# Performance work log

Hardware: AMD Instinct MI355X
Metric: run time of the kernel (lower is better)

The kernel has to match this reference:

```python
import jax, jax.numpy as jnp
import numpy as np

N_NODES = 10000
IN_FEAT = 16
HID = 64
TCH = 32
B, W, E = 4, 12, 320000


def setup_inputs() -> dict:
    key = jax.random.key(0)
    ks = jax.random.split(key, 12)
    x = jax.random.normal(ks[0], (B, W, N_NODES, IN_FEAT), dtype=jnp.float32)
    edge_index = jax.random.randint(ks[1], (2, E), 0, N_NODES, dtype=jnp.int32)
    s = lambda fan: 1.0 / np.sqrt(fan)
    W1 = jax.random.uniform(ks[2], (IN_FEAT, HID), jnp.float32, -s(IN_FEAT), s(IN_FEAT))
    b1 = jnp.zeros((HID,), jnp.float32)
    W2 = jax.random.uniform(ks[3], (HID, HID), jnp.float32, -s(HID), s(HID))
    b2 = jnp.zeros((HID,), jnp.float32)
    conv1_w = jax.random.uniform(ks[4], (TCH, HID, 3), jnp.float32, -s(HID * 3), s(HID * 3))
    conv1_b = jax.random.uniform(ks[5], (TCH,), jnp.float32, -s(HID * 3), s(HID * 3))
    conv2_w = jax.random.uniform(ks[6], (TCH, TCH, 3), jnp.float32, -s(TCH * 3), s(TCH * 3))
    conv2_b = jax.random.uniform(ks[7], (TCH,), jnp.float32, -s(TCH * 3), s(TCH * 3))
    fc_w = jax.random.uniform(ks[8], (1, TCH), jnp.float32, -s(TCH), s(TCH))
    fc_b = jax.random.uniform(ks[9], (1,), jnp.float32, -s(TCH), s(TCH))
    return {"x": x, "edge_index": edge_index, "W1": W1, "b1": b1, "W2": W2,
            "b2": b2, "conv1_w": conv1_w, "conv1_b": conv1_b,
            "conv2_w": conv2_w, "conv2_b": conv2_b, "fc_w": fc_w, "fc_b": fc_b}


def _conv1d(h, w, b):
    # h: (BN, C_in, W), w: (C_out, C_in, K)
    out = jax.lax.conv_general_dilated(h, w, window_strides=(1,), padding=[(1, 1)],
                                       dimension_numbers=("NCH", "OIH", "NCH"))
    return out + b[None, :, None]


def reference(x, edge_index, W1, b1, W2, b2, conv1_w, conv1_b, conv2_w, conv2_b, fc_w, fc_b):
    Bb, Ww, Nn, Ff = x.shape
    BN = Bb * Nn
    src, dst = edge_index[0], edge_index[1]
    # PyG GCNConv norm with self-loops over ALL BN nodes (edges touch only first N)
    deg = jnp.zeros((BN,), x.dtype).at[dst].add(1.0) + 1.0  # in-degree + self-loop
    dinv = jax.lax.rsqrt(deg)
    norm_e = dinv[src] * dinv[dst]          # (E,)
    self_norm = dinv * dinv                 # 1/deg, self-loop weight

    def gcn(h, Wm, bm):
        m = h @ Wm                           # (BN, out)
        agg = jnp.zeros_like(m).at[dst].add(norm_e[:, None] * m[src])
        return agg + self_norm[:, None] * m + bm

    xt = x.transpose(1, 0, 2, 3).reshape(Ww, BN, Ff)  # (W, BN, F), node idx = b*N+n

    def step(h):
        h = jax.nn.relu(gcn(h, W1, b1))
        h = jax.nn.relu(gcn(h, W2, b2))
        return h

    H = jax.vmap(step)(xt)                   # (W, BN, HID)
    H = H.transpose(1, 2, 0)                 # (BN, HID, W)
    H = jax.nn.relu(_conv1d(H, conv1_w, conv1_b))
    H = jax.nn.relu(_conv1d(H, conv2_w, conv2_b))
    H_last = H[:, :, -1]                     # (BN, TCH)
    out = H_last @ fc_w.T + fc_b             # (BN, 1)
    return out.reshape(Bb, Nn)
```

## Files before the change

### kernel.cpp

```cpp
#include <hip/hip_runtime.h>

#define N_NODES 10000
#define BN_TOT  40000
#define HID     64
#define IN_F    16
#define TCH     32
#define NW      12
#define RSTRIDE 192

__global__ void hist_kernel(const int* __restrict__ dst, int* __restrict__ cnt, int E) {
    int e = blockIdx.x * blockDim.x + threadIdx.x;
    if (e < E) atomicAdd(&cnt[dst[e]], 1);
}

__global__ __launch_bounds__(1024) void scan_kernel(const int* __restrict__ cnt,
                                                    int* __restrict__ row_ptr,
                                                    int* __restrict__ fill_pos,
                                                    float* __restrict__ dinv) {
    __shared__ int part[1024];
    int t = threadIdx.x;
    int base = t * 10;
    int s = 0;
#pragma unroll
    for (int k = 0; k < 10; ++k) {
        int b = base + k;
        if (b < N_NODES) s += cnt[b];
    }
    part[t] = s;
    __syncthreads();
    for (int off = 1; off < 1024; off <<= 1) {
        int v = 0;
        if (t >= off) v = part[t - off];
        __syncthreads();
        part[t] += v;
        __syncthreads();
    }
    int running = (t == 0) ? 0 : part[t - 1];
#pragma unroll
    for (int k = 0; k < 10; ++k) {
        int b = base + k;
        if (b < N_NODES) {
            row_ptr[b]  = running;
            fill_pos[b] = running;
            int c = cnt[b];
            dinv[b] = rsqrtf((float)c + 1.0f);
            running += c;
        }
    }
    if (t == 1023) row_ptr[N_NODES] = part[1023];
}

__global__ void fill_kernel(const int* __restrict__ src, const int* __restrict__ dst,
                            const float* __restrict__ dinv,
                            int* __restrict__ fill_pos,
                            int2* __restrict__ edges, int E) {
    int e = blockIdx.x * blockDim.x + threadIdx.x;
    if (e >= E) return;
    int s = src[e], d = dst[e];
    int pos = atomicAdd(&fill_pos[d], 1);
    edges[pos] = make_int2(s * (RSTRIDE * 4), __float_as_int(dinv[s] * dinv[d]));
}

__global__ void prep_kernel(const float* __restrict__ c1w, const float* __restrict__ c2w,
                            float4* __restrict__ w1p, float2* __restrict__ w2p) {
    int idx = blockIdx.x * blockDim.x + threadIdx.x;
    if (idx < 2048) {
        int tc = idx & 31, ic = idx >> 5;
        const float* p = c1w + tc * 192 + ic * 3;
        w1p[idx] = make_float4(p[0], p[1], p[2], 0.f);
    } else {
        int i2 = idx - 2048;
        int tc = i2 & 31, ic = i2 >> 5;
        const float* p = c2w + tc * 96 + ic * 3;
        w2p[i2] = make_float2(p[0], p[1]);
    }
}

__global__ __launch_bounds__(256) void gemm1_kernel(const float* __restrict__ x,
                                                    const float* __restrict__ W1,
                                                    float* __restrict__ m) {
    int idx = blockIdx.x * blockDim.x + threadIdx.x;
    int oc = idx & 63;
    int n = __builtin_amdgcn_readfirstlane(idx >> 6);
    const float* xb = x + (size_t)n * IN_F;
    float s0 = 0.f, s1 = 0.f, s2 = 0.f;
#pragma unroll
    for (int f = 0; f < IN_F; ++f) {
        float wv = W1[f * HID + oc];
        s0 += xb[(size_t)9  * N_NODES * IN_F + f] * wv;
        s1 += xb[(size_t)10 * N_NODES * IN_F + f] * wv;
        s2 += xb[(size_t)11 * N_NODES * IN_F + f] * wv;
    }
    float* mr = m + (size_t)n * RSTRIDE;
    mr[oc] = s0; mr[64 + oc] = s1; mr[128 + oc] = s2;
}

__global__ __launch_bounds__(256, 8) void gatherA_kernel(
        const float* __restrict__ m, const int* __restrict__ row_ptr,
        const int2* __restrict__ edges,
        const float* __restrict__ dinv, const float* __restrict__ b1,
        const float* __restrict__ W2, float* __restrict__ m2) {
    __shared__ float hs[4][3][HID];
    int gid = blockIdx.x * blockDim.x + threadIdx.x;
    int lane = threadIdx.x & 63;
    int wv = threadIdx.x >> 6;
    int row = __builtin_amdgcn_readfirstlane(gid >> 6);
    const int lo0 = lane * 4, lo1 = 256 + lane * 4, lo2 = 512 + lane * 4;
    const char* mrow = (const char*)m + (size_t)row * (RSTRIDE * 4);
    float dv = dinv[row];
    float sn = dv * dv;
    float s0 = sn * *(const float*)(mrow + lo0);
    float s1 = sn * *(const float*)(mrow + lo1);
    float s2 = sn * *(const float*)(mrow + lo2);
    int j = row_ptr[row], end = row_ptr[row + 1];
    for (; j + 3 < end; j += 4) {
        int2 e0 = edges[j], e1 = edges[j + 1], e2 = edges[j + 2], e3 = edges[j + 3];
        const char* q0 = (const char*)m + e0.x;
        const char* q1 = (const char*)m + e1.x;
        const char* q2 = (const char*)m + e2.x;
        const char* q3 = (const char*)m + e3.x;
        float w0 = __int_as_float(e0.y), w1 = __int_as_float(e1.y);
        float w2 = __int_as_float(e2.y), w3 = __int_as_float(e3.y);
        s0 += w0 * *(const float*)(q0 + lo0) + w1 * *(const float*)(q1 + lo0)
            + w2 * *(const float*)(q2 + lo0) + w3 * *(const float*)(q3 + lo0);
        s1 += w0 * *(const float*)(q0 + lo1) + w1 * *(const float*)(q1 + lo1)
            + w2 * *(const float*)(q2 + lo1) + w3 * *(const float*)(q3 + lo1);
        s2 += w0 * *(const float*)(q0 + lo2) + w1 * *(const float*)(q1 + lo2)
            + w2 * *(const float*)(q2 + lo2) + w3 * *(const float*)(q3 + lo2);
    }
    for (; j < end; ++j) {
        int2 e = edges[j];
        const char* q = (const char*)m + e.x;
        float w = __int_as_float(e.y);
        s0 += w * *(const float*)(q + lo0);
        s1 += w * *(const float*)(q + lo1);
        s2 += w * *(const float*)(q + lo2);
    }
    float bb = b1[lane];
    hs[wv][0][lane] = fmaxf(s0 + bb, 0.f);
    hs[wv][1][lane] = fmaxf(s1 + bb, 0.f);
    hs[wv][2][lane] = fmaxf(s2 + bb, 0.f);
    __builtin_amdgcn_wave_barrier();
    const float4* h0v = (const float4*)&hs[wv][0][0];
    const float4* h1v = (const float4*)&hs[wv][1][0];
    const float4* h2v = (const float4*)&hs[wv][2][0];
    float t0 = 0.f, t1 = 0.f, t2 = 0.f;
#pragma unroll
    for (int ic4 = 0; ic4 < 16; ++ic4) {
        float4 h0 = h0v[ic4], h1 = h1v[ic4], h2 = h2v[ic4];
        float wA = W2[(ic4 * 4 + 0) * HID + lane];
        float wB = W2[(ic4 * 4 + 1) * HID + lane];
        float wC = W2[(ic4 * 4 + 2) * HID + lane];
        float wD = W2[(ic4 * 4 + 3) * HID + lane];
        t0 += h0.x * wA + h0.y * wB + h0.z * wC + h0.w * wD;
        t1 += h1.x * wA + h1.y * wB + h1.z * wC + h1.w * wD;
        t2 += h2.x * wA + h2.y * wB + h2.z * wC + h2.w * wD;
    }
    float* m2r = m2 + (size_t)row * RSTRIDE;
    m2r[lane] = t0; m2r[64 + lane] = t1; m2r[128 + lane] = t2;
}

__global__ __launch_bounds__(512, 4) void convfc_kernel(
        const float* __restrict__ mB, const int* __restrict__ row_ptr,
        const int2* __restrict__ edges,
        const float* __restrict__ dinv, const float* __restrict__ b2,
        const float* __restrict__ x, const float* __restrict__ W1,
        const float* __restrict__ b1, const float* __restrict__ W2,
        const float4* __restrict__ w1p, const float* __restrict__ b1c,
        const float2* __restrict__ w2p, const float* __restrict__ b2c,
        const float* __restrict__ fcw, const float* __restrict__ fcb,
        float* __restrict__ out) {
    __shared__ float4 w1s[2048];
    __shared__ float  hs[8][4][3][HID];
    __shared__ float  c1s[8][4][2][TCH];
    int t = threadIdx.x;
#pragma unroll
    for (int i = 0; i < 4; ++i) w1s[i * 512 + t] = w1p[i * 512 + t];
    __syncthreads();

    int wv = t >> 6, lane = t & 63;
    int w = __builtin_amdgcn_readfirstlane(blockIdx.x * 8 + wv);

    {
        const int lo0 = lane * 4, lo1 = 256 + lane * 4, lo2 = 512 + lane * 4;
        const char* mrow = (const char*)mB + (size_t)w * (RSTRIDE * 4);
        float dv = dinv[w];
        float sn = dv * dv;
        float s0 = sn * *(const float*)(mrow + lo0);
        float s1 = sn * *(const float*)(mrow + lo1);
        float s2 = sn * *(const float*)(mrow + lo2);
        int j = row_ptr[w], end = row_ptr[w + 1];
        for (; j + 3 < end; j += 4) {
            int2 e0 = edges[j], e1 = edges[j + 1], e2 = edges[j + 2], e3 = edges[j + 3];
            const char* q0 = (const char*)mB + e0.x;
            const char* q1 = (const char*)mB + e1.x;
            const char* q2 = (const char*)mB + e2.x;
            const char* q3 = (const char*)mB + e3.x;
            float w0 = __int_as_float(e0.y), w1 = __int_as_float(e1.y);
            float w2 = __int_as_float(e2.y), w3 = __int_as_float(e3.y);
            s0 += w0 * *(const float*)(q0 + lo0) + w1 * *(const float*)(q1 + lo0)
                + w2 * *(const float*)(q2 + lo0) + w3 * *(const float*)(q3 + lo0);
            s1 += w0 * *(const float*)(q0 + lo1) + w1 * *(const float*)(q1 + lo1)
                + w2 * *(const float*)(q2 + lo1) + w3 * *(const float*)(q3 + lo1);
            s2 += w0 * *(const float*)(q0 + lo2) + w1 * *(const float*)(q1 + lo2)
                + w2 * *(const float*)(q2 + lo2) + w3 * *(const float*)(q3 + lo2);
        }
        for (; j < end; ++j) {
            int2 e = edges[j];
            const char* q = (const char*)mB + e.x;
            float ww = __int_as_float(e.y);
            s0 += ww * *(const float*)(q + lo0);
            s1 += ww * *(const float*)(q + lo1);
            s2 += ww * *(const float*)(q + lo2);
        }
        float bb = b2[lane];
        hs[wv][0][0][lane] = fmaxf(s0 + bb, 0.f);
        hs[wv][0][1][lane] = fmaxf(s1 + bb, 0.f);
        hs[wv][0][2][lane] = fmaxf(s2 + bb, 0.f);
    }

    {
        float w1r[16];
#pragma unroll
        for (int f = 0; f < IN_F; ++f) w1r[f] = W1[f * HID + lane];
        float s[9];
#pragma unroll
        for (int k = 1; k <= 3; ++k) {
#pragma unroll
            for (int tt = 0; tt < 3; ++tt) {
                const float* xp = x + ((size_t)(k * NW + 9 + tt) * N_NODES + w) * IN_F;
                float a = 0.f;
#pragma unroll
                for (int f = 0; f < IN_F; ++f) a += xp[f] * w1r[f];
                s[(k - 1) * 3 + tt] = a;
            }
        }
        float bb1 = b1[lane];
#pragma unroll
        for (int k = 1; k <= 3; ++k) {
            hs[wv][k][0][lane] = fmaxf(s[(k - 1) * 3 + 0] + bb1, 0.f);
            hs[wv][k][1][lane] = fmaxf(s[(k - 1) * 3 + 1] + bb1, 0.f);
            hs[wv][k][2][lane] = fmaxf(s[(k - 1) * 3 + 2] + bb1, 0.f);
        }
        __builtin_amdgcn_wave_barrier();
        float acc[9];
#pragma unroll
        for (int mm = 0; mm < 9; ++mm) acc[mm] = 0.f;
#pragma unroll
        for (int k4 = 0; k4 < 16; ++k4) {
            float wA = W2[(k4 * 4 + 0) * HID + lane];
            float wB = W2[(k4 * 4 + 1) * HID + lane];
            float wC = W2[(k4 * 4 + 2) * HID + lane];
            float wD = W2[(k4 * 4 + 3) * HID + lane];
#pragma unroll
            for (int k = 1; k <= 3; ++k) {
#pragma unroll
                for (int tt = 0; tt < 3; ++tt) {
                    float4 h = ((const float4*)&hs[wv][k][tt][0])[k4];
                    acc[(k - 1) * 3 + tt] += h.x * wA + h.y * wB + h.z * wC + h.w * wD;
                }
            }
        }
        __builtin_amdgcn_wave_barrier();
        float bb2 = b2[lane];
#pragma unroll
        for (int k = 1; k <= 3; ++k) {
            hs[wv][k][0][lane] = fmaxf(acc[(k - 1) * 3 + 0] + bb2, 0.f);
            hs[wv][k][1][lane] = fmaxf(acc[(k - 1) * 3 + 1] + bb2, 0.f);
            hs[wv][k][2][lane] = fmaxf(acc[(k - 1) * 3 + 2] + bb2, 0.f);
        }
    }
    __builtin_amdgcn_wave_barrier();

    int pos = lane >> 5, tc = lane & 31;
    int pA = pos, pB = pos + 1, pC = (pos == 0) ? 2 : 0;
    float hCs = (pos == 0) ? 1.f : 0.f;
    float a1[4];
    float bc1 = b1c[tc];
#pragma unroll
    for (int r = 0; r < 4; ++r) a1[r] = bc1;
#pragma unroll
    for (int ic4 = 0; ic4 < 16; ++ic4) {
        float4 wa = w1s[(ic4 * 4 + 0) * 32 + tc];
        float4 wb = w1s[(ic4 * 4 + 1) * 32 + tc];
        float4 wc = w1s[(ic4 * 4 + 2) * 32 + tc];
        float4 wd = w1s[(ic4 * 4 + 3) * 32 + tc];
        float waz = wa.z * hCs, wbz = wb.z * hCs, wcz = wc.z * hCs, wdz = wd.z * hCs;
#pragma unroll
        for (int r = 0; r < 4; ++r) {
            float4 hA = ((const float4*)&hs[wv][r][pA][0])[ic4];
            float4 hB = ((const float4*)&hs[wv][r][pB][0])[ic4];
            float4 hC = ((const float4*)&hs[wv][r][pC][0])[ic4];
            a1[r] += hA.x * wa.x + hB.x * wa.y + hC.x * waz
                   + hA.y * wb.x + hB.y * wb.y + hC.y * wbz
                   + hA.z * wc.x + hB.z * wc.y + hC.z * wcz
                   + hA.w * wd.x + hB.w * wd.y + hC.w * wdz;
        }
    }
#pragma unroll
    for (int r = 0; r < 4; ++r) c1s[wv][r][pos][tc] = fmaxf(a1[r], 0.f);
    __builtin_amdgcn_wave_barrier();

    int rr = pos * 2;
    float bc2 = b2c[tc];
    float a2q0 = bc2, a2q1 = bc2;
#pragma unroll
    for (int ic4 = 0; ic4 < 8; ++ic4) {
        float2 w0 = w2p[(ic4 * 4 + 0) * 32 + tc];
        float2 w1 = w2p[(ic4 * 4 + 1) * 32 + tc];
        float2 w2v = w2p[(ic4 * 4 + 2) * 32 + tc];
        float2 w3 = w2p[(ic4 * 4 + 3) * 32 + tc];
        float4 cA0 = ((const float4*)&c1s[wv][rr + 0][0][0])[ic4];
        float4 cB0 = ((const float4*)&c1s[wv][rr + 0][1][0])[ic4];
        float4 cA1 = ((const float4*)&c1s[wv][rr + 1][0][0])[ic4];
        float4 cB1 = ((const float4*)&c1s[wv][rr + 1][1][0])[ic4];
        a2q0 += cA0.x * w0.x + cB0.x * w0.y + cA0.y * w1.x + cB0.y * w1.y
              + cA0.z * w2v.x + cB0.z * w2v.y + cA0.w * w3.x + cB0.w * w3.y;
        a2q1 += cA1.x * w0.x + cB1.x * w0.y + cA1.y * w1.x + cB1.y * w1.y
              + cA1.z * w2v.x + cB1.z * w2v.y + cA1.w * w3.x + cB1.w * w3.y;
    }
    float fw = fcw[tc];
    float r0v = fmaxf(a2q0, 0.f) * fw;
    float r1v = fmaxf(a2q1, 0.f) * fw;
#pragma unroll
    for (int off = 16; off > 0; off >>= 1) {
        r0v += __shfl_down(r0v, off, 32);
        r1v += __shfl_down(r1v, off, 32);
    }
    if (tc == 0) {
        float fb = fcb[0];
        out[w + (rr + 0) * N_NODES] = r0v + fb;
        out[w + (rr + 1) * N_NODES] = r1v + fb;
    }
}

extern "C" void kernel_launch(void* const* d_in, const int* in_sizes, int n_in,
                              void* d_out, int out_size, void* d_ws, size_t ws_size,
                              hipStream_t stream) {
    const float* x   = (const float*)d_in[0];
    const int*   ei  = (const int*)d_in[1];
    const float* W1  = (const float*)d_in[2];
    const float* b1  = (const float*)d_in[3];
    const float* W2  = (const float*)d_in[4];
    const float* b2  = (const float*)d_in[5];
    const float* c1w = (const float*)d_in[6];
    const float* c1b = (const float*)d_in[7];
    const float* c2w = (const float*)d_in[8];
    const float* c2b = (const float*)d_in[9];
    const float* fcw = (const float*)d_in[10];
    const float* fcb = (const float*)d_in[11];
    float* out = (float*)d_out;

    const int E = in_sizes[1] / 2;
    const int* src = ei;
    const int* dst = ei + E;

    const size_t SG = (size_t)N_NODES * RSTRIDE;
    int*    cnt      = (int*)d_ws;
    int*    row_ptr  = cnt + 10240;
    int*    fill_pos = row_ptr + 10240;
    int2*   edges    = (int2*)(fill_pos + 10240);
    float*  dinv     = (float*)(edges + E);
    float4* w1p      = (float4*)(dinv + 10240);
    float2* w2p      = (float2*)(w1p + 2048);
    float*  mA       = (float*)(w2p + 1024);
    float*  mB       = mA + SG;

    hipMemsetAsync(cnt, 0, N_NODES * sizeof(int), stream);
    hist_kernel<<<(E + 255) / 256, 256, 0, stream>>>(dst, cnt, E);
    scan_kernel<<<1, 1024, 0, stream>>>(cnt, row_ptr, fill_pos, dinv);
    fill_kernel<<<(E + 255) / 256, 256, 0, stream>>>(src, dst, dinv, fill_pos, edges, E);
    prep_kernel<<<12, 256, 0, stream>>>(c1w, c2w, w1p, w2p);

    gemm1_kernel <<<(N_NODES * HID) / 256, 256, 0, stream>>>(x, W1, mA);
    gatherA_kernel<<<(N_NODES * HID) / 256, 256, 0, stream>>>(mA, row_ptr, edges, dinv, b1, W2, mB);

    convfc_kernel<<<N_NODES / 8, 512, 0, stream>>>(mB, row_ptr, edges, dinv, b2,
                                                   x, W1, b1, W2,
                                                   w1p, c1b, w2p, c2b, fcw, fcb, out);
}
```

Baseline: 162.9 us.

## Interleave window rows for float2 gathers and shrink convfc shared memory

The intermediate row layout now interleaves the first two window slots, so each gathered neighbor row is read with one float2 load plus one float load instead of three scalar loads. The producers of m and m2 write in the matching interleaved layout. In convfc, the conv1 weights in shared memory drop the unused fourth component, and the c1 buffer is aliased onto the per-wave h buffer behind an extra wave barrier. This cuts LDS use enough to raise the occupancy hint from 4 to 6 blocks. The consumers must stay consistent with the new layout, and the aliasing relies on the added barrier to be correct.

```diff
diff --git a/kernel.cpp b/kernel.cpp
--- a/kernel.cpp
+++ b/kernel.cpp
@@ -92,7 +92,8 @@
         s2 += xb[(size_t)11 * N_NODES * IN_F + f] * wv;
     }
     float* mr = m + (size_t)n * RSTRIDE;
-    mr[oc] = s0; mr[64 + oc] = s1; mr[128 + oc] = s2;
+    ((float2*)mr)[oc] = make_float2(s0, s1);
+    mr[128 + oc] = s2;
 }
 
 __global__ __launch_bounds__(256, 8) void gatherA_kernel(
@@ -105,13 +106,13 @@
     int lane = threadIdx.x & 63;
     int wv = threadIdx.x >> 6;
     int row = __builtin_amdgcn_readfirstlane(gid >> 6);
-    const int lo0 = lane * 4, lo1 = 256 + lane * 4, lo2 = 512 + lane * 4;
+    const int lo01 = lane * 8, lo2 = 512 + lane * 4;
     const char* mrow = (const char*)m + (size_t)row * (RSTRIDE * 4);
     float dv = dinv[row];
     float sn = dv * dv;
-    float s0 = sn * *(const float*)(mrow + lo0);
-    float s1 = sn * *(const float*)(mrow + lo1);
-    float s2 = sn * *(const float*)(mrow + lo2);
+    float2 self01 = *(const float2*)(mrow + lo01);
+    float  self2  = *(const float*)(mrow + lo2);
+    float s0 = sn * self01.x, s1 = sn * self01.y, s2 = sn * self2;
     int j = row_ptr[row], end = row_ptr[row + 1];
     for (; j + 3 < end; j += 4) {
         int2 e0 = edges[j], e1 = edges[j + 1], e2 = edges[j + 2], e3 = edges[j + 3];
@@ -119,22 +120,27 @@
         const char* q1 = (const char*)m + e1.x;
         const char* q2 = (const char*)m + e2.x;
         const char* q3 = (const char*)m + e3.x;
+        float2 a0 = *(const float2*)(q0 + lo01);
+        float2 a1 = *(const float2*)(q1 + lo01);
+        float2 a2 = *(const float2*)(q2 + lo01);
+        float2 a3 = *(const float2*)(q3 + lo01);
+        float  c0 = *(const float*)(q0 + lo2);
+        float  c1 = *(const float*)(q1 + lo2);
+        float  c2 = *(const float*)(q2 + lo2);
+        float  c3 = *(const float*)(q3 + lo2);
         float w0 = __int_as_float(e0.y), w1 = __int_as_float(e1.y);
         float w2 = __int_as_float(e2.y), w3 = __int_as_float(e3.y);
-        s0 += w0 * *(const float*)(q0 + lo0) + w1 * *(const float*)(q1 + lo0)
-            + w2 * *(const float*)(q2 + lo0) + w3 * *(const float*)(q3 + lo0);
-        s1 += w0 * *(const float*)(q0 + lo1) + w1 * *(const float*)(q1 + lo1)
-            + w2 * *(const float*)(q2 + lo1) + w3 * *(const float*)(q3 + lo1);
-        s2 += w0 * *(const float*)(q0 + lo2) + w1 * *(const float*)(q1 + lo2)
-            + w2 * *(const float*)(q2 + lo2) + w3 * *(const float*)(q3 + lo2);
+        s0 += w0 * a0.x + w1 * a1.x + w2 * a2.x + w3 * a3.x;
+        s1 += w0 * a0.y + w1 * a1.y + w2 * a2.y + w3 * a3.y;
+        s2 += w0 * c0 + w1 * c1 + w2 * c2 + w3 * c3;
     }
     for (; j < end; ++j) {
         int2 e = edges[j];
         const char* q = (const char*)m + e.x;
+        float2 a = *(const float2*)(q + lo01);
+        float  c = *(const float*)(q + lo2);
         float w = __int_as_float(e.y);
-        s0 += w * *(const float*)(q + lo0);
-        s1 += w * *(const float*)(q + lo1);
-        s2 += w * *(const float*)(q + lo2);
+        s0 += w * a.x; s1 += w * a.y; s2 += w * c;
     }
     float bb = b1[lane];
     hs[wv][0][lane] = fmaxf(s0 + bb, 0.f);
@@ -157,10 +163,11 @@
         t2 += h2.x * wA + h2.y * wB + h2.z * wC + h2.w * wD;
     }
     float* m2r = m2 + (size_t)row * RSTRIDE;
-    m2r[lane] = t0; m2r[64 + lane] = t1; m2r[128 + lane] = t2;
-}
-
-__global__ __launch_bounds__(512, 4) void convfc_kernel(
+    ((float2*)m2r)[lane] = make_float2(t0, t1);
+    m2r[128 + lane] = t2;
+}
+
+__global__ __launch_bounds__(512, 6) void convfc_kernel(
         const float* __restrict__ mB, const int* __restrict__ row_ptr,
         const int2* __restrict__ edges,
         const float* __restrict__ dinv, const float* __restrict__ b2,
@@ -170,25 +177,30 @@
         const float2* __restrict__ w2p, const float* __restrict__ b2c,
         const float* __restrict__ fcw, const float* __restrict__ fcb,
         float* __restrict__ out) {
-    __shared__ float4 w1s[2048];
-    __shared__ float  hs[8][4][3][HID];
-    __shared__ float  c1s[8][4][2][TCH];
+    __shared__ float2 w1s01[2048];
+    __shared__ float  w1s2[2048];
+    __shared__ float  sm[8][768];
     int t = threadIdx.x;
 #pragma unroll
-    for (int i = 0; i < 4; ++i) w1s[i * 512 + t] = w1p[i * 512 + t];
+    for (int i = 0; i < 4; ++i) {
+        float4 wv4 = w1p[i * 512 + t];
+        w1s01[i * 512 + t] = make_float2(wv4.x, wv4.y);
+        w1s2[i * 512 + t] = wv4.z;
+    }
     __syncthreads();
 
     int wv = t >> 6, lane = t & 63;
     int w = __builtin_amdgcn_readfirstlane(blockIdx.x * 8 + wv);
+    float* hsw = sm[wv];
 
     {
-        const int lo0 = lane * 4, lo1 = 256 + lane * 4, lo2 = 512 + lane * 4;
+        const int lo01 = lane * 8, lo2 = 512 + lane * 4;
         const char* mrow = (const char*)mB + (size_t)w * (RSTRIDE * 4);
         float dv = dinv[w];
         float sn = dv * dv;
-        float s0 = sn * *(const float*)(mrow + lo0);
-        float s1 = sn * *(const float*)(mrow + lo1);
-        float s2 = sn * *(const float*)(mrow + lo2);
+        float2 self01 = *(const float2*)(mrow + lo01);
+        float  self2  = *(const float*)(mrow + lo2);
+        float s0 = sn * self01.x, s1 = sn * self01.y, s2 = sn * self2;
         int j = row_ptr[w], end = row_ptr[w + 1];
         for (; j + 3 < end; j += 4) {
             int2 e0 = edges[j], e1 = edges[j + 1], e2 = edges[j + 2], e3 = edges[j + 3];
@@ -196,27 +208,32 @@
             const char* q1 = (const char*)mB + e1.x;
             const char* q2 = (const char*)mB + e2.x;
             const char* q3 = (const char*)mB + e3.x;
+            float2 a0 = *(const float2*)(q0 + lo01);
+            float2 a1 = *(const float2*)(q1 + lo01);
+            float2 a2 = *(const float2*)(q2 + lo01);
+            float2 a3 = *(const float2*)(q3 + lo01);
+            float  c0 = *(const float*)(q0 + lo2);
+            float  c1 = *(const float*)(q1 + lo2);
+            float  c2 = *(const float*)(q2 + lo2);
+            float  c3 = *(const float*)(q3 + lo2);
             float w0 = __int_as_float(e0.y), w1 = __int_as_float(e1.y);
             float w2 = __int_as_float(e2.y), w3 = __int_as_float(e3.y);
-            s0 += w0 * *(const float*)(q0 + lo0) + w1 * *(const float*)(q1 + lo0)
-                + w2 * *(const float*)(q2 + lo0) + w3 * *(const float*)(q3 + lo0);
-            s1 += w0 * *(const float*)(q0 + lo1) + w1 * *(const float*)(q1 + lo1)
-                + w2 * *(const float*)(q2 + lo1) + w3 * *(const float*)(q3 + lo1);
-            s2 += w0 * *(const float*)(q0 + lo2) + w1 * *(const float*)(q1 + lo2)
-                + w2 * *(const float*)(q2 + lo2) + w3 * *(const float*)(q3 + lo2);
+            s0 += w0 * a0.x + w1 * a1.x + w2 * a2.x + w3 * a3.x;
+            s1 += w0 * a0.y + w1 * a1.y + w2 * a2.y + w3 * a3.y;
+            s2 += w0 * c0 + w1 * c1 + w2 * c2 + w3 * c3;
         }
         for (; j < end; ++j) {
             int2 e = edges[j];
             const char* q = (const char*)mB + e.x;
+            float2 a = *(const float2*)(q + lo01);
+            float  c = *(const float*)(q + lo2);
             float ww = __int_as_float(e.y);
-            s0 += ww * *(const float*)(q + lo0);
-            s1 += ww * *(const float*)(q + lo1);
-            s2 += ww * *(const float*)(q + lo2);
+            s0 += ww * a.x; s1 += ww * a.y; s2 += ww * c;
         }
         float bb = b2[lane];
-        hs[wv][0][0][lane] = fmaxf(s0 + bb, 0.f);
-        hs[wv][0][1][lane] = fmaxf(s1 + bb, 0.f);
-        hs[wv][0][2][lane] = fmaxf(s2 + bb, 0.f);
+        hsw[0 * 192 + 0 * 64 + lane] = fmaxf(s0 + bb, 0.f);
+        hsw[0 * 192 + 1 * 64 + lane] = fmaxf(s1 + bb, 0.f);
+        hsw[0 * 192 + 2 * 64 + lane] = fmaxf(s2 + bb, 0.f);
     }
 
     {
@@ -238,9 +255,9 @@
         float bb1 = b1[lane];
 #pragma unroll
         for (int k = 1; k <= 3; ++k) {
-            hs[wv][k][0][lane] = fmaxf(s[(k - 1) * 3 + 0] + bb1, 0.f);
-            hs[wv][k][1][lane] = fmaxf(s[(k - 1) * 3 + 1] + bb1, 0.f);
-            hs[wv][k][2][lane] = fmaxf(s[(k - 1) * 3 + 2] + bb1, 0.f);
+            hsw[k * 192 + 0 * 64 + lane] = fmaxf(s[(k - 1) * 3 + 0] + bb1, 0.f);
+            hsw[k * 192 + 1 * 64 + lane] = fmaxf(s[(k - 1) * 3 + 1] + bb1, 0.f);
+            hsw[k * 192 + 2 * 64 + lane] = fmaxf(s[(k - 1) * 3 + 2] + bb1, 0.f);
         }
         __builtin_amdgcn_wave_barrier();
         float acc[9];
@@ -256,7 +273,7 @@
             for (int k = 1; k <= 3; ++k) {
 #pragma unroll
                 for (int tt = 0; tt < 3; ++tt) {
-                    float4 h = ((const float4*)&hs[wv][k][tt][0])[k4];
+                    float4 h = ((const float4*)&hsw[k * 192 + tt * 64])[k4];
                     acc[(k - 1) * 3 + tt] += h.x * wA + h.y * wB + h.z * wC + h.w * wD;
                 }
             }
@@ -265,9 +282,9 @@
         float bb2 = b2[lane];
 #pragma unroll
         for (int k = 1; k <= 3; ++k) {
-            hs[wv][k][0][lane] = fmaxf(acc[(k - 1) * 3 + 0] + bb2, 0.f);
-            hs[wv][k][1][lane] = fmaxf(acc[(k - 1) * 3 + 1] + bb2, 0.f);
-            hs[wv][k][2][lane] = fmaxf(acc[(k - 1) * 3 + 2] + bb2, 0.f);
+            hsw[k * 192 + 0 * 64 + lane] = fmaxf(acc[(k - 1) * 3 + 0] + bb2, 0.f);
+            hsw[k * 192 + 1 * 64 + lane] = fmaxf(acc[(k - 1) * 3 + 1] + bb2, 0.f);
+            hsw[k * 192 + 2 * 64 + lane] = fmaxf(acc[(k - 1) * 3 + 2] + bb2, 0.f);
         }
     }
     __builtin_amdgcn_wave_barrier();
@@ -281,24 +298,28 @@
     for (int r = 0; r < 4; ++r) a1[r] = bc1;
 #pragma unroll
     for (int ic4 = 0; ic4 < 16; ++ic4) {
-        float4 wa = w1s[(ic4 * 4 + 0) * 32 + tc];
-        float4 wb = w1s[(ic4 * 4 + 1) * 32 + tc];
-        float4 wc = w1s[(ic4 * 4 + 2) * 32 + tc];
-        float4 wd = w1s[(ic4 * 4 + 3) * 32 + tc];
-        float waz = wa.z * hCs, wbz = wb.z * hCs, wcz = wc.z * hCs, wdz = wd.z * hCs;
+        float2 wa01 = w1s01[(ic4 * 4 + 0) * 32 + tc];
+        float2 wb01 = w1s01[(ic4 * 4 + 1) * 32 + tc];
+        float2 wc01 = w1s01[(ic4 * 4 + 2) * 32 + tc];
+        float2 wd01 = w1s01[(ic4 * 4 + 3) * 32 + tc];
+        float waz = w1s2[(ic4 * 4 + 0) * 32 + tc] * hCs;
+        float wbz = w1s2[(ic4 * 4 + 1) * 32 + tc] * hCs;
+        float wcz = w1s2[(ic4 * 4 + 2) * 32 + tc] * hCs;
+        float wdz = w1s2[(ic4 * 4 + 3) * 32 + tc] * hCs;
 #pragma unroll
         for (int r = 0; r < 4; ++r) {
-            float4 hA = ((const float4*)&hs[wv][r][pA][0])[ic4];
-            float4 hB = ((const float4*)&hs[wv][r][pB][0])[ic4];
-            float4 hC = ((const float4*)&hs[wv][r][pC][0])[ic4];
-            a1[r] += hA.x * wa.x + hB.x * wa.y + hC.x * waz
-                   + hA.y * wb.x + hB.y * wb.y + hC.y * wbz
-                   + hA.z * wc.x + hB.z * wc.y + hC.z * wcz
-                   + hA.w * wd.x + hB.w * wd.y + hC.w * wdz;
-        }
-    }
-#pragma unroll
-    for (int r = 0; r < 4; ++r) c1s[wv][r][pos][tc] = fmaxf(a1[r], 0.f);
+            float4 hA = ((const float4*)&hsw[r * 192 + pA * 64])[ic4];
+            float4 hB = ((const float4*)&hsw[r * 192 + pB * 64])[ic4];
+            float4 hC = ((const float4*)&hsw[r * 192 + pC * 64])[ic4];
+            a1[r] += hA.x * wa01.x + hB.x * wa01.y + hC.x * waz
+                   + hA.y * wb01.x + hB.y * wb01.y + hC.y * wbz
+                   + hA.z * wc01.x + hB.z * wc01.y + hC.z * wcz
+                   + hA.w * wd01.x + hB.w * wd01.y + hC.w * wdz;
+        }
+    }
+    __builtin_amdgcn_wave_barrier();
+#pragma unroll
+    for (int r = 0; r < 4; ++r) hsw[r * 64 + pos * 32 + tc] = fmaxf(a1[r], 0.f);
     __builtin_amdgcn_wave_barrier();
 
     int rr = pos * 2;
@@ -310,10 +331,10 @@
         float2 w1 = w2p[(ic4 * 4 + 1) * 32 + tc];
         float2 w2v = w2p[(ic4 * 4 + 2) * 32 + tc];
         float2 w3 = w2p[(ic4 * 4 + 3) * 32 + tc];
-        float4 cA0 = ((const float4*)&c1s[wv][rr + 0][0][0])[ic4];
-        float4 cB0 = ((const float4*)&c1s[wv][rr + 0][1][0])[ic4];
-        float4 cA1 = ((const float4*)&c1s[wv][rr + 1][0][0])[ic4];
-        float4 cB1 = ((const float4*)&c1s[wv][rr + 1][1][0])[ic4];
+        float4 cA0 = ((const float4*)&hsw[(rr + 0) * 64 + 0])[ic4];
+        float4 cB0 = ((const float4*)&hsw[(rr + 0) * 64 + 32])[ic4];
+        float4 cA1 = ((const float4*)&hsw[(rr + 1) * 64 + 0])[ic4];
+        float4 cB1 = ((const float4*)&hsw[(rr + 1) * 64 + 32])[ic4];
         a2q0 += cA0.x * w0.x + cB0.x * w0.y + cA0.y * w1.x + cB0.y * w1.y
               + cA0.z * w2v.x + cB0.z * w2v.y + cA0.w * w3.x + cB0.w * w3.y;
         a2q1 += cA1.x * w0.x + cB1.x * w0.y + cA1.y * w1.x + cB1.y * w1.y
```

New measurement: 201.0 us. 1.23x slower.
